# Kernel tuning notes

Hardware: AMD Instinct MI355X
Metric: run time of the kernel (lower is better)

The kernel has to match this reference:

```python
import math
import jax, jax.numpy as jnp
import numpy as np

B = 32        # number of graphs
MAXN = 4096   # nodes per graph (all graphs full)
C = 256       # emb_size_atom
NSEEDS = 409  # int(number_atoms * 0.1)
TOTAL = B * MAXN
INV06 = 1.0 / 0.6
INV_SQRT2 = 1.0 / math.sqrt(2.0)

def scaled_silu(x):
    return jax.nn.silu(x) * INV06

def dense(x, W):
    # Dense(bias=False, activation='silu') == ScaledSiLU(x @ W^T)
    return scaled_silu(x @ W.T)

def res_layer(x, W1, W2):
    return (x + dense(dense(x, W1), W2)) * INV_SQRT2

def layer_norm(x, g, b, eps=1e-5):
    m = jnp.mean(x, -1, keepdims=True)
    v = jnp.var(x, -1, keepdims=True)
    return (x - m) * jax.lax.rsqrt(v + eps) * g + b

def split_heads(x, H):
    # torch.cat(x.split(dV//H, 2), dim=0): head-major stacking on batch axis
    b, n, d = x.shape
    return x.reshape(b, n, H, d // H).transpose(2, 0, 1, 3).reshape(H * b, n, d // H)

def merge_heads(x, H, b):
    _, n, dh = x.shape
    return x.reshape(H, b, n, dh).transpose(1, 2, 0, 3).reshape(b, n, H * dh)

def base_mha(Q, K, Wq, bq, Wk, bk, Wv, bv, Wo, bo, g0, b0, g1, b1, H, mask=None):
    dV = Wq.shape[0]
    Q_ = split_heads(Q @ Wq.T + bq, H)
    K_ = split_heads(K @ Wk.T + bk, H)
    V_ = split_heads(K @ Wv.T + bv, H)
    score = jnp.einsum('bqd,bkd->bqk', Q_, K_) * (1.0 / math.sqrt(dV))
    if mask is not None:
        score = score + jnp.tile(mask, (H, 1, 1))
    A = jax.nn.softmax(score, axis=1)  # FAITHFUL: softmax over the QUERY axis (dim=1 in source)
    out = merge_heads(Q_ + jnp.einsum('bqk,bkd->bqd', A, V_), H, Q.shape[0])
    out = layer_norm(out, g0, b0)
    out = out + jax.nn.relu(out @ Wo.T + bo)
    out = layer_norm(out, g1, b1)
    return out, A

def to_dense_batch(x, batch):
    total = x.shape[0]
    counts = jax.ops.segment_sum(jnp.ones((total,), jnp.int32), batch, num_segments=B)
    offsets = jnp.concatenate([jnp.zeros((1,), jnp.int32), jnp.cumsum(counts)[:-1]])
    pos = jnp.arange(total) - offsets[batch]  # position of each node within its graph
    dense_x = jnp.zeros((B, MAXN, x.shape[-1]), x.dtype).at[batch, pos].set(x)
    omask = jnp.zeros((B, MAXN), bool).at[batch, pos].set(True)
    return dense_x, omask, pos

def _forward(h, batch_seg, W_pre1, W_pre2, S, pWq, pbq, pWk, pbk, pWv, pbv, pWo, pbo, pg0, pb0, pg1, pb1, iWq, ibq, iWk, ibk, iWv, ibv, iWo, ibo, ig0, ib0, ig1, ib1, W_head, W_r1a, W_r1b, W_r2a, W_r2b):
    hres = res_layer(h, W_pre1, W_pre2)
    dx, omask, pos = to_dense_batch(hres, batch_seg)
    mask = jnp.where(omask, 0.0, -1e9).astype(hres.dtype)[:, None, :]  # [B,1,MAXN]
    Q = jnp.tile(S, (B, 1, 1))  # learned seeds [B,NSEEDS,C]
    NAs, A1 = base_mha(Q, dx, pWq, pbq, pWk, pbk, pWv, pbv, pWo, pbo, pg0, pb0, pg1, pb1, 1, mask)
    NAs, _ = base_mha(NAs, NAs, iWq, ibq, iWk, ibk, iWv, ibv, iWo, ibo, ig0, ib0, ig1, ib1, 2, None)
    h_back = jnp.einsum('bsn,bsc->bnc', A1, NAs)  # project back: A1^T @ NAs
    h_up = h_back[batch_seg, pos]                 # flatten back to [TOTAL, C]
    h_up = dense(h_up, W_head)
    h_up = res_layer(h_up, W_r1a, W_r1b)
    h_up = res_layer(h_up, W_r2a, W_r2b)
    return h_up

def setup_inputs() -> dict:
    key = jax.random.key(0)
    ks = jax.random.split(key, 20)
    sc = 1.0 / math.sqrt(C)
    w = lambda k: jax.random.normal(k, (C, C), jnp.float32) * sc
    zb = jnp.zeros((C,), jnp.float32)
    og = jnp.ones((C,), jnp.float32)
    return {
        'h': jax.random.normal(ks[0], (TOTAL, C), jnp.float32),
        'batch_seg': jnp.arange(TOTAL, dtype=jnp.int32) // MAXN,
        'W_pre1': w(ks[1]), 'W_pre2': w(ks[2]),
        'S': jax.random.normal(ks[3], (1, NSEEDS, C), jnp.float32) * math.sqrt(2.0 / (NSEEDS + C)),
        'pWq': w(ks[4]), 'pbq': zb, 'pWk': w(ks[5]), 'pbk': zb,
        'pWv': w(ks[6]), 'pbv': zb, 'pWo': w(ks[7]), 'pbo': zb,
        'pg0': og, 'pb0': zb, 'pg1': og, 'pb1': zb,
        'iWq': w(ks[8]), 'ibq': zb, 'iWk': w(ks[9]), 'ibk': zb,
        'iWv': w(ks[10]), 'ibv': zb, 'iWo': w(ks[11]), 'ibo': zb,
        'ig0': og, 'ib0': zb, 'ig1': og, 'ib1': zb,
        'W_head': w(ks[12]),
        'W_r1a': w(ks[13]), 'W_r1b': w(ks[14]),
        'W_r2a': w(ks[15]), 'W_r2b': w(ks[16]),
    }

def reference(h, batch_seg, W_pre1, W_pre2, S, pWq, pbq, pWk, pbk, pWv, pbv, pWo, pbo, pg0, pb0, pg1, pb1, iWq, ibq, iWk, ibk, iWv, ibv, iWo, ibo, ig0, ib0, ig1, ib1, W_head, W_r1a, W_r1b, W_r2a, W_r2b):
    return _forward(h, batch_seg, W_pre1, W_pre2, S, pWq, pbq, pWk, pbk, pWv, pbv, pWo, pbo, pg0, pb0, pg1, pb1, iWq, ibq, iWk, ibk, iWv, ibv, iWo, ibo, ig0, ib0, ig1, ib1, W_head, W_r1a, W_r1b, W_r2a, W_r2b)
```

## Files before the change

kernel.cpp:

```cpp
#include <hip/hip_runtime.h>


#define BM 128
#define BN 128
#define BKT 32
#define PKM 132
#define XS  264
#define NJOBS 33

typedef __attribute__((ext_vector_type(8))) __bf16 bf16x8;
typedef __attribute__((ext_vector_type(4))) __bf16 bf16x4;
typedef __attribute__((ext_vector_type(4))) float  f32x4;

struct CastJobs {
    const float* src[NJOBS];
    __bf16*      dst[NJOBS];
    long         n[NJOBS];
    int          startBlk[NJOBS];
};

__global__ void cast_many_k(CastJobs J)
{
    int b = blockIdx.x;
    int j = 0;
#pragma unroll
    for (int t = 0; t < NJOBS; t++) { if (J.startBlk[t] <= b) j = t; }
    long idx = ((long)(b - J.startBlk[j]) * 256 + threadIdx.x) * 4;
    if (idx < J.n[j]) {
        f32x4 v = *(const f32x4*)(J.src[j] + idx);
        bf16x4 o;
        o[0] = (__bf16)v[0]; o[1] = (__bf16)v[1];
        o[2] = (__bf16)v[2]; o[3] = (__bf16)v[3];
        *(bf16x4*)(J.dst[j] + idx) = o;
    }
}

__device__ __forceinline__ void gload_lds16(const __bf16* g, __bf16* l)
{
    __builtin_amdgcn_global_load_lds(
        (const __attribute__((address_space(1))) void*)g,
        (__attribute__((address_space(3))) void*)l, 16, 0, 0);
}

__device__ __forceinline__ float ssilu(float v)
{
    float e = __expf(-fabsf(v));
    float sig = (v >= 0.0f) ? 1.0f / (1.0f + e) : e / (1.0f + e);
    return v * sig * 1.6666666666666667f;
}

__device__ __forceinline__ void chain_gemm(const __bf16* __restrict__ Xl,
                                           const __bf16* __restrict__ W,
                                           f32x4 (&acc)[4][4],
                                           int wn, int l15, int lq)
{
#pragma unroll
    for (int i = 0; i < 4; i++)
#pragma unroll
        for (int j = 0; j < 4; j++)
#pragma unroll
            for (int r = 0; r < 4; r++) acc[i][j][r] = 0.0f;
#pragma unroll
    for (int k0 = 0; k0 < 8; k0++) {
        bf16x8 af[4], bfr[4];
#pragma unroll
        for (int i = 0; i < 4; i++)
            af[i] = *(const bf16x8*)(Xl + (i * 16 + l15) * XS + k0 * 32 + lq * 8);
#pragma unroll
        for (int j = 0; j < 4; j++)
            bfr[j] = *(const bf16x8*)(W + (long)(wn + j * 16 + l15) * 256 + k0 * 32 + lq * 8);
#pragma unroll
        for (int i = 0; i < 4; i++)
#pragma unroll
            for (int j = 0; j < 4; j++)
                acc[i][j] = __builtin_amdgcn_mfma_f32_16x16x32_bf16(af[i], bfr[j], acc[i][j], 0, 0, 0);
    }
}

__device__ __forceinline__ void epi_to_lds(const f32x4 (&acc)[4][4],
                                           __bf16* __restrict__ dst,
                                           const __bf16* __restrict__ resL,
                                           int wn, int l15, int lq)
{
#pragma unroll
    for (int i = 0; i < 4; i++)
#pragma unroll
        for (int j = 0; j < 4; j++) {
            int col = wn + j * 16 + l15;
#pragma unroll
            for (int r = 0; r < 4; r++) {
                int row = i * 16 + lq * 4 + r;
                float v = ssilu(acc[i][j][r]);
                if (resL) v = ((float)resL[row * XS + col] + v) * 0.70710678118654752f;
                dst[row * XS + col] = (__bf16)v;
            }
        }
}

__launch_bounds__(256, 2)
__global__ void fuse_front_k(const __bf16* __restrict__ h,
                             const __bf16* __restrict__ Wp1,
                             const __bf16* __restrict__ Wp2,
                             const __bf16* __restrict__ pWk, const __bf16* __restrict__ pbk,
                             const __bf16* __restrict__ pWv, const __bf16* __restrict__ pbv,
                             __bf16* __restrict__ Kb, __bf16* __restrict__ Vt)
{
    __shared__ __align__(16) __bf16 B0[64 * XS];
    __shared__ __align__(16) __bf16 B1[64 * XS];
    const int tid = threadIdx.x, lane = tid & 63, wv = tid >> 6;
    const int wn = wv * 64, l15 = lane & 15, lq = lane >> 4;
    const long row0 = (long)blockIdx.x * 64;

#pragma unroll
    for (int i = 0; i < 8; i++) {
        int v = tid + i * 256;
        int r = v >> 5, kc = (v & 31) * 8;
        *(bf16x8*)(B0 + r * XS + kc) = *(const bf16x8*)(h + (row0 + r) * 256 + kc);
    }
    __syncthreads();

    f32x4 acc[4][4];
    chain_gemm(B0, Wp1, acc, wn, l15, lq);
    epi_to_lds(acc, B1, nullptr, wn, l15, lq);
    __syncthreads();

    chain_gemm(B1, Wp2, acc, wn, l15, lq);
    __syncthreads();
    epi_to_lds(acc, B1, B0, wn, l15, lq);
    __syncthreads();

    chain_gemm(B1, pWk, acc, wn, l15, lq);
#pragma unroll
    for (int i = 0; i < 4; i++)
#pragma unroll
        for (int j = 0; j < 4; j++) {
            int col = wn + j * 16 + l15;
            float bc = (float)pbk[col];
#pragma unroll
            for (int r = 0; r < 4; r++) {
                int row = i * 16 + lq * 4 + r;
                Kb[(row0 + row) * 256 + col] = (__bf16)(acc[i][j][r] + bc);
            }
        }

    chain_gemm(B1, pWv, acc, wn, l15, lq);
    {
        long g   = row0 >> 12;
        long n0g = row0 & 4095;
#pragma unroll
        for (int i = 0; i < 4; i++)
#pragma unroll
            for (int j = 0; j < 4; j++) {
                int col = wn + j * 16 + l15;
                float bc = (float)pbv[col];
                long nb = n0g + i * 16 + lq * 4;
                bf16x4 ov;
#pragma unroll
                for (int r = 0; r < 4; r++) ov[r] = (__bf16)(acc[i][j][r] + bc);
                *(bf16x4*)(Vt + ((g * 256 + col) << 12) + nb) = ov;
            }
    }
}

__launch_bounds__(256, 2)
__global__ void fuse_tail_k(const __bf16* __restrict__ HB,
                            const __bf16* __restrict__ Wh,
                            const __bf16* __restrict__ W1a, const __bf16* __restrict__ W1b,
                            const __bf16* __restrict__ W2a, const __bf16* __restrict__ W2b,
                            float* __restrict__ OUT)
{
    __shared__ __align__(16) __bf16 B0[64 * XS];
    __shared__ __align__(16) __bf16 B1[64 * XS];
    const int tid = threadIdx.x, lane = tid & 63, wv = tid >> 6;
    const int wn = wv * 64, l15 = lane & 15, lq = lane >> 4;
    const long row0 = (long)blockIdx.x * 64;

#pragma unroll
    for (int i = 0; i < 8; i++) {
        int v = tid + i * 256;
        int r = v >> 5, kc = (v & 31) * 8;
        *(bf16x8*)(B0 + r * XS + kc) = *(const bf16x8*)(HB + (row0 + r) * 256 + kc);
    }
    __syncthreads();

    f32x4 acc[4][4];
    chain_gemm(B0, Wh, acc, wn, l15, lq);
    epi_to_lds(acc, B1, nullptr, wn, l15, lq);
    __syncthreads();

    chain_gemm(B1, W1a, acc, wn, l15, lq);
    epi_to_lds(acc, B0, nullptr, wn, l15, lq);
    __syncthreads();

    chain_gemm(B0, W1b, acc, wn, l15, lq);
    __syncthreads();
    epi_to_lds(acc, B0, B1, wn, l15, lq);
    __syncthreads();

    chain_gemm(B0, W2a, acc, wn, l15, lq);
    epi_to_lds(acc, B1, nullptr, wn, l15, lq);
    __syncthreads();

    chain_gemm(B1, W2b, acc, wn, l15, lq);
#pragma unroll
    for (int i = 0; i < 4; i++)
#pragma unroll
        for (int j = 0; j < 4; j++) {
            int col = wn + j * 16 + l15;
#pragma unroll
            for (int r = 0; r < 4; r++) {
                int row = i * 16 + lq * 4 + r;
                float v = ssilu(acc[i][j][r]);
                v = ((float)B0[row * XS + col] + v) * 0.70710678118654752f;
                OUT[(row0 + row) * 256 + col] = v;
            }
        }
}

template<int TRANS>
__device__ __forceinline__ bool stage_load(bf16x8 (&rv)[2], __bf16* __restrict__ lds,
                                           const __bf16* __restrict__ G,
                                           int ld, int r0, int Rg,
                                           int k0, int K, int tid)
{
    if (TRANS == 0) {
        const bool fast = ((ld & 7) == 0) && (r0 + BM <= Rg) && (k0 + BKT <= K);
        if (fast) {
#pragma unroll
            for (int i = 0; i < 2; i++) {
                int v = tid + i * 256;
                int r = v >> 2, kc = (v & 3) * 8;
                gload_lds16(G + (long)(r0 + r) * ld + (k0 + kc), lds + v * 8);
            }
            return true;
        }
#pragma unroll
        for (int i = 0; i < 2; i++) {
            int v = tid + i * 256;
            int r = v >> 2, kc = (v & 3) * 8;
            int gm = r0 + r, gk = k0 + kc;
            bf16x8 val;
#pragma unroll
            for (int j = 0; j < 8; j++) val[j] = (__bf16)0.0f;
            if (gm < Rg) {
                if (((ld & 7) == 0) && (gk + 8 <= K)) {
                    val = *(const bf16x8*)(G + (long)gm * ld + gk);
                } else {
#pragma unroll
                    for (int j = 0; j < 8; j++)
                        if (gk + j < K) val[j] = G[(long)gm * ld + gk + j];
                }
            }
            rv[i] = val;
        }
        return false;
    } else {
#pragma unroll
        for (int i = 0; i < 2; i++) {
            int v = tid + i * 256;
            int kk = v >> 4;
            int mc = (v & 15) * 8;
            int gk = k0 + kk, gm = r0 + mc;
            bf16x8 val;
#pragma unroll
            for (int j = 0; j < 8; j++) val[j] = (__bf16)0.0f;
            if (gk < K) {
                if (((ld & 7) == 0) && (gm + 8 <= Rg)) {
                    val = *(const bf16x8*)(G + (long)gk * ld + gm);
                } else {
#pragma unroll
                    for (int j = 0; j < 8; j++)
                        if (gm + j < Rg) val[j] = G[(long)gk * ld + gm + j];
                }
            }
            rv[i] = val;
        }
        return false;
    }
}

template<int TRANS>
__device__ __forceinline__ void stage_write(const bf16x8 (&rv)[2], __bf16* __restrict__ lds,
                                            int tid, bool fast)
{
    if (TRANS == 0) {
        if (fast) return;
#pragma unroll
        for (int i = 0; i < 2; i++)
            *(bf16x8*)(lds + (tid + i * 256) * 8) = rv[i];
    } else {
#pragma unroll
        for (int i = 0; i < 2; i++) {
            int v = tid + i * 256;
            int kk = v >> 4, mc = (v & 15) * 8;
            bf16x4 lo, hi;
            lo[0] = rv[i][0]; lo[1] = rv[i][1]; lo[2] = rv[i][2]; lo[3] = rv[i][3];
            hi[0] = rv[i][4]; hi[1] = rv[i][5]; hi[2] = rv[i][6]; hi[3] = rv[i][7];
            *(bf16x4*)(lds + kk * PKM + mc)     = lo;
            *(bf16x4*)(lds + kk * PKM + mc + 4) = hi;
        }
    }
}

template<int AT, int BT>
__device__ __forceinline__ void frag_mfma(const __bf16* __restrict__ Ac,
                                          const __bf16* __restrict__ Bc,
                                          f32x4 (&acc)[4][4],
                                          int wm, int wn, int l15, int lq)
{
    bf16x8 af[4], bfr[4];
    if (AT == 0) {
#pragma unroll
        for (int i = 0; i < 4; i++)
            af[i] = *(const bf16x8*)(Ac + (wm + i * 16 + l15) * BKT + lq * 8);
    } else {
#pragma unroll
        for (int i = 0; i < 4; i++) {
            int m = wm + i * 16 + l15;
#pragma unroll
            for (int j = 0; j < 8; j++) af[i][j] = Ac[(lq * 8 + j) * PKM + m];
        }
    }
    if (BT == 1) {
#pragma unroll
        for (int j = 0; j < 4; j++)
            bfr[j] = *(const bf16x8*)(Bc + (wn + j * 16 + l15) * BKT + lq * 8);
    } else {
#pragma unroll
        for (int j = 0; j < 4; j++) {
            int n = wn + j * 16 + l15;
#pragma unroll
            for (int jj = 0; jj < 8; jj++) bfr[j][jj] = Bc[(lq * 8 + jj) * PKM + n];
        }
    }
#pragma unroll
    for (int i = 0; i < 4; i++)
#pragma unroll
        for (int j = 0; j < 4; j++)
            acc[i][j] = __builtin_amdgcn_mfma_f32_16x16x32_bf16(af[i], bfr[j], acc[i][j], 0, 0, 0);
}

template<int AT, int BT, int PIPE>
__launch_bounds__(256, 2)
__global__ void gemm_k(const __bf16* __restrict__ A, long aLo, long aHi, int lda, int Ms,
                       const __bf16* __restrict__ Bm, long bLo, long bHi, int ldb, int Ns,
                       const __bf16* __restrict__ bias,
                       const __bf16* __restrict__ res, long rLo, long rHi, int ldr, int resMode,
                       float* __restrict__ outF, __bf16* __restrict__ outB,
                       long oLo, long oHi, int ldo, int storeT,
                       int M, int N, int K, float oscale, int act)
{
    constexpr int BTT = (BT == 1) ? 0 : 1;
    constexpr int NBUF = PIPE ? 2 : 1;
    __shared__ __align__(16) __bf16 As[NBUF * BKT * PKM];
    __shared__ __align__(16) __bf16 Bs[NBUF * BKT * PKM];

    const int tid = threadIdx.x;
    const int z = blockIdx.z;
    const long zl = (long)(z & 31), zh = (long)(z >> 5);
    const __bf16* Ab = A + zl * aLo + zh * aHi;
    const __bf16* Bb = Bm + zl * bLo + zh * bHi;
    const int m0 = blockIdx.x * BM;
    const int n0 = blockIdx.y * BN;

    f32x4 acc[4][4];
#pragma unroll
    for (int i = 0; i < 4; i++)
#pragma unroll
        for (int j = 0; j < 4; j++)
#pragma unroll
            for (int r = 0; r < 4; r++) acc[i][j][r] = 0.0f;

    const int wv = tid >> 6;
    const int lane = tid & 63;
    const int wm = (wv >> 1) * 64;
    const int wn = (wv & 1) * 64;
    const int l15 = lane & 15;
    const int lq  = lane >> 4;

    if (PIPE == 0) {
        for (int k0 = 0; k0 < K; k0 += BKT) {
            bf16x8 ra[2], rb[2];
            bool fa = stage_load<AT>(ra, As, Ab, lda, m0, Ms, k0, K, tid);
            bool fb = stage_load<BTT>(rb, Bs, Bb, ldb, n0, Ns, k0, K, tid);
            stage_write<AT>(ra, As, tid, fa);
            stage_write<BTT>(rb, Bs, tid, fb);
            __syncthreads();
            frag_mfma<AT, BT>(As, Bs, acc, wm, wn, l15, lq);
            __syncthreads();
        }
    } else {
        constexpr int TSZ = BKT * PKM;
        const int nt = (K + BKT - 1) / BKT;
        bf16x8 ra[2], rb[2];
        bool fa = stage_load<AT>(ra, As, Ab, lda, m0, Ms, 0, K, tid);
        bool fb = stage_load<BTT>(rb, Bs, Bb, ldb, n0, Ns, 0, K, tid);
        stage_write<AT>(ra, As, tid, fa);
        stage_write<BTT>(rb, Bs, tid, fb);
        __syncthreads();
        int cur = 0;
        for (int t = 0; t < nt; t++) {
            const bool nxt = (t + 1 < nt);
            if (nxt) {
                fa = stage_load<AT>(ra, As + (cur ^ 1) * TSZ, Ab, lda, m0, Ms, (t + 1) * BKT, K, tid);
                fb = stage_load<BTT>(rb, Bs + (cur ^ 1) * TSZ, Bb, ldb, n0, Ns, (t + 1) * BKT, K, tid);
            }
            frag_mfma<AT, BT>(As + cur * TSZ, Bs + cur * TSZ, acc, wm, wn, l15, lq);
            if (nxt) {
                stage_write<AT>(ra, As + (cur ^ 1) * TSZ, tid, fa);
                stage_write<BTT>(rb, Bs + (cur ^ 1) * TSZ, tid, fb);
                __syncthreads();
                cur ^= 1;
            }
        }
    }

    const __bf16* Rb = res ? (res + zl * rLo + zh * rHi) : (const __bf16*)nullptr;
    const long ob = zl * oLo + zh * oHi;
#pragma unroll
    for (int i = 0; i < 4; i++) {
#pragma unroll
        for (int j = 0; j < 4; j++) {
            int col = n0 + wn + j * 16 + l15;
            if (col >= N) continue;
            float bcol = bias ? (float)bias[col] : 0.0f;
            int row0 = m0 + wm + i * 16 + lq * 4;
            if (!storeT) {
#pragma unroll
                for (int r = 0; r < 4; r++) {
                    int row = row0 + r;
                    if (row >= M) continue;
                    float v = acc[i][j][r] * oscale + bcol;
                    if (act == 1) v = ssilu(v);
                    else if (act == 2) v = fmaxf(v, 0.0f);
                    if (resMode) {
                        float rv = (float)Rb[(long)row * ldr + col];
                        v = (resMode == 1) ? (rv + v) * 0.70710678118654752f : (rv + v);
                    }
                    long oi = ob + (long)row * ldo + col;
                    if (outF) outF[oi] = v;
                    else      outB[oi] = (__bf16)v;
                }
            } else {
                if (row0 + 3 < M) {
                    bf16x4 rv4;
                    if (resMode) rv4 = *(const bf16x4*)(Rb + (long)col * ldr + row0);
                    float vs[4];
#pragma unroll
                    for (int r = 0; r < 4; r++) {
                        float v = acc[i][j][r] * oscale + bcol;
                        if (act == 1) v = ssilu(v);
                        else if (act == 2) v = fmaxf(v, 0.0f);
                        if (resMode) {
                            float rv = (float)rv4[r];
                            v = (resMode == 1) ? (rv + v) * 0.70710678118654752f : (rv + v);
                        }
                        vs[r] = v;
                    }
                    if (outF) {
                        f32x4 o4; o4[0] = vs[0]; o4[1] = vs[1]; o4[2] = vs[2]; o4[3] = vs[3];
                        *(f32x4*)(outF + ob + (long)col * ldo + row0) = o4;
                    } else {
                        bf16x4 ov;
                        ov[0] = (__bf16)vs[0]; ov[1] = (__bf16)vs[1];
                        ov[2] = (__bf16)vs[2]; ov[3] = (__bf16)vs[3];
                        *(bf16x4*)(outB + ob + (long)col * ldo + row0) = ov;
                    }
                } else {
#pragma unroll
                    for (int r = 0; r < 4; r++) {
                        int row = row0 + r;
                        if (row >= M) continue;
                        float v = acc[i][j][r] * oscale + bcol;
                        if (act == 1) v = ssilu(v);
                        else if (act == 2) v = fmaxf(v, 0.0f);
                        if (resMode) {
                            float rv = (float)Rb[(long)col * ldr + row];
                            v = (resMode == 1) ? (rv + v) * 0.70710678118654752f : (rv + v);
                        }
                        if (outF) outF[ob + (long)col * ldo + row] = v;
                        else      outB[ob + (long)col * ldo + row] = (__bf16)v;
                    }
                }
            }
        }
    }
}

__global__ void reduce4_k(const float* __restrict__ P, const __bf16* __restrict__ Qp,
                          __bf16* __restrict__ out)
{
    long idx = (long)blockIdx.x * 256 + threadIdx.x;
    long g = idx / (409 * 64);
    long r = idx - g * (409 * 64);
    long s = r >> 6;
    int  c4 = (int)(r & 63) * 4;
    long base = (g * 409 + s) * 256 + c4;
    const long SP = 32L * 409 * 256;
    f32x4 a0 = *(const f32x4*)(P + base);
    f32x4 a1 = *(const f32x4*)(P + base + SP);
    f32x4 a2 = *(const f32x4*)(P + base + 2 * SP);
    f32x4 a3 = *(const f32x4*)(P + base + 3 * SP);
    bf16x4 q = *(const bf16x4*)(Qp + s * 256 + c4);
    bf16x4 o;
#pragma unroll
    for (int k = 0; k < 4; k++)
        o[k] = (__bf16)(a0[k] + a1[k] + a2[k] + a3[k] + (float)q[k]);
    *(bf16x4*)(out + base) = o;
}

__global__ void rowsoftmax_k(const float* __restrict__ S, __bf16* __restrict__ A,
                             long rows, int L, int ldS, int ldA, int Lw)
{
    long row = (long)blockIdx.x * 4 + (threadIdx.x >> 6);
    if (row >= rows) return;
    int lane = threadIdx.x & 63;
    const float* Sr = S + row * (long)ldS;
    float v[7];
    int cnt = 0;
    for (int q = lane; q < L; q += 64) v[cnt++] = Sr[q];
    float m = -3.0e38f;
    for (int c = 0; c < cnt; c++) m = fmaxf(m, v[c]);
#pragma unroll
    for (int off = 32; off > 0; off >>= 1) m = fmaxf(m, __shfl_xor(m, off));
    float s = 0.0f;
    for (int c = 0; c < cnt; c++) s += __expf(v[c] - m);
#pragma unroll
    for (int off = 32; off > 0; off >>= 1) s += __shfl_xor(s, off);
    float inv = 1.0f / s;
    cnt = 0;
    for (int q = lane; q < Lw; q += 64) {
        float o = 0.0f;
        if (q < L) { o = __expf(v[cnt] - m) * inv; cnt++; }
        A[row * (long)ldA + q] = (__bf16)o;
    }
}

__global__ void ln_k(const __bf16* __restrict__ X, __bf16* __restrict__ Y,
                     const __bf16* __restrict__ gamma, const __bf16* __restrict__ beta,
                     int rows)
{
    int row = blockIdx.x * 4 + (threadIdx.x >> 6);
    if (row >= rows) return;
    int lane = threadIdx.x & 63;
    bf16x4 xv = *(const bf16x4*)(X + (long)row * 256 + lane * 4);
    float v0 = (float)xv[0], v1 = (float)xv[1], v2 = (float)xv[2], v3 = (float)xv[3];
    float s = v0 + v1 + v2 + v3;
#pragma unroll
    for (int off = 32; off > 0; off >>= 1) s += __shfl_xor(s, off);
    float mean = s * (1.0f / 256.0f);
    float d0 = v0 - mean, d1 = v1 - mean, d2 = v2 - mean, d3 = v3 - mean;
    float q = d0 * d0 + d1 * d1 + d2 * d2 + d3 * d3;
#pragma unroll
    for (int off = 32; off > 0; off >>= 1) q += __shfl_xor(q, off);
    float sc = rsqrtf(q * (1.0f / 256.0f) + 1e-5f);
    bf16x4 gv = *(const bf16x4*)(gamma + lane * 4);
    bf16x4 bv = *(const bf16x4*)(beta + lane * 4);
    bf16x4 ov;
    ov[0] = (__bf16)(d0 * sc * (float)gv[0] + (float)bv[0]);
    ov[1] = (__bf16)(d1 * sc * (float)gv[1] + (float)bv[1]);
    ov[2] = (__bf16)(d2 * sc * (float)gv[2] + (float)bv[2]);
    ov[3] = (__bf16)(d3 * sc * (float)gv[3] + (float)bv[3]);
    *(bf16x4*)(Y + (long)row * 256 + lane * 4) = ov;
}

__global__ void sentinel_k(float* out, long n)
{
    long i = (long)blockIdx.x * blockDim.x + threadIdx.x;
    if (i < n) out[i] = 12345.0f;
}

static void G(hipStream_t st, int AT, int BT,
              const __bf16* A, long aLo, long aHi, int lda, int Ms,
              const __bf16* B, long bLo, long bHi, int ldb, int Ns,
              const __bf16* bias,
              const __bf16* res, long rLo, long rHi, int ldr, int resMode,
              float* outF, __bf16* outB, long oLo, long oHi, int ldo, int storeT,
              int M, int N, int K, int Z, float oscale, int act)
{
    dim3 grid((M + BM - 1) / BM, (N + BN - 1) / BN, Z), blk(256, 1, 1);
#define GARGS A, aLo, aHi, lda, Ms, B, bLo, bHi, ldb, Ns, bias, res, rLo, rHi, ldr, resMode, \
              outF, outB, oLo, oHi, ldo, storeT, M, N, K, oscale, act
    if (AT == 0 && BT == 1) {
        gemm_k<0, 1, 0><<<grid, blk, 0, st>>>(GARGS);
    } else if (AT == 0 && BT == 0) {
        if (K >= 512) gemm_k<0, 0, 1><<<grid, blk, 0, st>>>(GARGS);
        else          gemm_k<0, 0, 0><<<grid, blk, 0, st>>>(GARGS);
    } else {
        gemm_k<1, 0, 0><<<grid, blk, 0, st>>>(GARGS);
    }
#undef GARGS
}

extern "C" void kernel_launch(void* const* d_in, const int* in_sizes, int n_in,
                              void* d_out, int out_size, void* d_ws, size_t ws_size,
                              hipStream_t stream)
{
    (void)in_sizes; (void)n_in;
    float* OUT = (float*)d_out;

    const int TOT = 131072, NC = 256, NS = 409, MX = 4096;
    const int NSP = 416;
    const int NSB = 32 * NS;
    const long NTC = (long)TOT * NC;
    const int GCH = 4;

    static const int  pidx[NJOBS] = {0,2,3,4,5,6,7,8,9,10,11,12,13,14,15,16,
                                     17,18,19,20,21,22,23,24,25,26,27,28,29,30,31,32,33};
    static const long pn[NJOBS]   = {33554432,65536,65536,104704,
                                     65536,256,65536,256,65536,256,65536,256,
                                     256,256,256,256,
                                     65536,256,65536,256,65536,256,65536,256,
                                     256,256,256,256,
                                     65536,65536,65536,65536,65536};
    long ptot = 0;
    for (int j = 0; j < NJOBS; j++) ptot += pn[j];

    char* w = (char*)d_ws;
    size_t off = 0;
    auto take = [&](size_t bytes) -> char* {
        char* p = w + off;
        off += (bytes + 255) & ~(size_t)255;
        return p;
    };
    char* pblk = take((size_t)ptot * 2);
    char* reg0 = take((size_t)64 * NS * NSP * 4);
    char* reg1 = take((size_t)32 * MX * NSP * 2);
    char* reg2 = take((size_t)NTC * 2);
    char* reg3 = take((size_t)NTC * 2);
    __bf16* QP  = (__bf16*)take((size_t)NS * NC * 2);
    __bf16* sb0 = (__bf16*)take((size_t)NSB * NC * 2);
    __bf16* sb1 = (__bf16*)take((size_t)NSB * NC * 2);
    __bf16* sb2 = (__bf16*)take((size_t)NSB * NC * 2);
    __bf16* sb3 = (__bf16*)take((size_t)NSB * NC * 2);
    __bf16* sb4 = (__bf16*)take((size_t)NSB * NC * 2);
    __bf16* sb5 = (__bf16*)take((size_t)NSB * NC * 2);

    if (off > ws_size) {
        long n = out_size;
        sentinel_k<<<(int)((n + 255) / 256), 256, 0, stream>>>(OUT, n);
        return;
    }

    CastJobs J;
    __bf16* P[NJOBS];
    {
        long cum = 0;
        int blk = 0;
        for (int j = 0; j < NJOBS; j++) {
            J.src[j] = (const float*)d_in[pidx[j]];
            P[j] = (__bf16*)pblk + cum;
            J.dst[j] = P[j];
            J.n[j] = pn[j];
            J.startBlk[j] = blk;
            blk += (int)((pn[j] + 1023) / 1024);
            cum += pn[j];
        }
        cast_many_k<<<blk, 256, 0, stream>>>(J);
    }
    const __bf16 *hB = P[0], *Wpre1 = P[1], *Wpre2 = P[2], *Sseed = P[3];
    const __bf16 *pWq = P[4], *pbq = P[5], *pWk = P[6], *pbk = P[7];
    const __bf16 *pWv = P[8], *pbv = P[9], *pWo = P[10], *pbo = P[11];
    const __bf16 *pg0 = P[12], *pb0 = P[13], *pg1 = P[14], *pb1 = P[15];
    const __bf16 *iWq = P[16], *ibq = P[17], *iWk = P[18], *ibk = P[19];
    const __bf16 *iWv = P[20], *ibv = P[21], *iWo = P[22], *ibo = P[23];
    const __bf16 *ig0 = P[24], *ib0 = P[25], *ig1 = P[26], *ib1 = P[27];
    const __bf16 *Whead = P[28], *Wr1a = P[29], *Wr1b = P[30];
    const __bf16 *Wr2a = P[31], *Wr2b = P[32];

    float*  STs = (float*)reg0;
    float*  S2T = (float*)reg0;
    __bf16* A1T = (__bf16*)reg1;
    __bf16* Kb  = (__bf16*)reg2;
    float*  PP  = (float*)reg2;
    __bf16* HB  = (__bf16*)reg2;
    __bf16* Vt  = (__bf16*)reg3;
    __bf16* A2T = (__bf16*)reg3;

    fuse_front_k<<<dim3(TOT / 64), 256, 0, stream>>>(hB, Wpre1, Wpre2,
                                                     pWk, pbk, pWv, pbv, Kb, Vt);
    G(stream, 0, 1, Sseed, 0, 0, 256, NS, pWq, 0, 0, 256, 256, pbq,
      nullptr, 0, 0, 0, 0, nullptr, QP, 0, 0, 256, 0, NS, 256, 256, 1, 1.0f, 0);
    for (int c = 0; c < 32 / GCH; c++) {
        const __bf16* Kc = Kb + (size_t)c * GCH * MX * NC;
        G(stream, 0, 1, Kc, (long)MX * NC, 0, 256, MX, QP, 0, 0, 256, NS, nullptr,
          nullptr, 0, 0, 0, 0, STs, nullptr, (long)MX * NSP, 0, NSP, 0,
          MX, NS, 256, GCH, 0.0625f, 0);
        rowsoftmax_k<<<dim3(GCH * MX / 4), 256, 0, stream>>>(
            STs, A1T + (size_t)c * GCH * MX * NSP, (long)GCH * MX, NS, NSP, NSP, NSP);
    }
    G(stream, 0, 0, Vt, (long)NC * MX, 1024, MX, NC,
      A1T, (long)MX * NSP, 1024L * NSP, NSP, NSP, nullptr,
      nullptr, 0, 0, 0, 0, PP, nullptr, (long)NS * NC, 32L * NS * NC, NC, 1,
      NC, NS, 1024, 128, 1.0f, 0);
    reduce4_k<<<dim3((unsigned)((32L * NS * 64) / 256)), 256, 0, stream>>>(PP, QP, sb0);
    ln_k<<<dim3(NSB / 4), 256, 0, stream>>>(sb0, sb1, pg0, pb0, NSB);
    G(stream, 0, 1, sb1, 0, 0, 256, NSB, pWo, 0, 0, 256, 256, pbo,
      sb1, 0, 0, 256, 2, nullptr, sb2, 0, 0, 256, 0, NSB, 256, 256, 1, 1.0f, 2);
    ln_k<<<dim3(NSB / 4), 256, 0, stream>>>(sb2, sb0, pg1, pb1, NSB);
    G(stream, 0, 1, sb0, 0, 0, 256, NSB, iWq, 0, 0, 256, 256, ibq,
      nullptr, 0, 0, 0, 0, nullptr, sb1, 0, 0, 256, 0, NSB, 256, 256, 1, 1.0f, 0);
    G(stream, 0, 1, sb0, 0, 0, 256, NSB, iWk, 0, 0, 256, 256, ibk,
      nullptr, 0, 0, 0, 0, nullptr, sb2, 0, 0, 256, 0, NSB, 256, 256, 1, 1.0f, 0);
    G(stream, 0, 1, sb0, 0, 0, 256, NSB, iWv, 0, 0, 256, 256, ibv,
      nullptr, 0, 0, 0, 0, nullptr, sb3, 0, 0, 256, 0, NSB, 256, 256, 1, 1.0f, 0);
    G(stream, 0, 1, sb2, (long)NS * NC, 128, 256, NS, sb1, (long)NS * NC, 128, 256, NS, nullptr,
      nullptr, 0, 0, 0, 0, S2T, nullptr, (long)NS * NSP, 32L * NS * NSP, NSP, 0,
      NS, NS, 128, 64, 0.0625f, 0);
    rowsoftmax_k<<<dim3(64 * NS / 4), 256, 0, stream>>>(S2T, A2T, 64L * NS, NS, NSP, NSP, NSP);
    G(stream, 1, 0, A2T, (long)NS * NSP, 32L * NS * NSP, NSP, NSP,
      sb3, (long)NS * NC, 128, 256, 128, nullptr,
      sb1, (long)NS * NC, 128, 256, 2, nullptr, sb4, (long)NS * NC, 128, 256, 0,
      NS, 128, NS, 64, 1.0f, 0);
    ln_k<<<dim3(NSB / 4), 256, 0, stream>>>(sb4, sb5, ig0, ib0, NSB);
    G(stream, 0, 1, sb5, 0, 0, 256, NSB, iWo, 0, 0, 256, 256, ibo,
      sb5, 0, 0, 256, 2, nullptr, sb4, 0, 0, 256, 0, NSB, 256, 256, 1, 1.0f, 2);
    ln_k<<<dim3(NSB / 4), 256, 0, stream>>>(sb4, sb1, ig1, ib1, NSB);
    G(stream, 0, 0, A1T, (long)MX * NSP, 0, NSP, MX, sb1, (long)NS * NC, 0, 256, 256, nullptr,
      nullptr, 0, 0, 0, 0, nullptr, HB, (long)MX * NC, 0, 256, 0, MX, 256, 416, 32, 1.0f, 0);
    fuse_tail_k<<<dim3(TOT / 64), 256, 0, stream>>>(HB, Whead, Wr1a, Wr1b,
                                                    Wr2a, Wr2b, OUT);
}
```

Baseline: 1.483 ms.

## Transpose chain GEMM operands for vectorized epilogues and register-held residuals

Adds a transposed chain GEMM variant where weights are the A operand, so each lane's accumulator holds four consecutive output columns. Epilogues can then use packed bf16x4 LDS and global stores and f32x4 output writes instead of scalar stores. Residuals in the head kernel are kept in registers rather than reread from LDS, which removes one barrier and an in-place residual pass. ScaledSiLU is simplified to a single exp plus a hardware reciprocal, which can lose accuracy or overflow for large negative inputs. The extra register arrays could raise register pressure under the launch bounds of two blocks per SIMD.

```diff
diff --git a/kernel.cpp b/kernel.cpp
--- a/kernel.cpp
+++ b/kernel.cpp
@@ -44,9 +44,36 @@
 
 __device__ __forceinline__ float ssilu(float v)
 {
-    float e = __expf(-fabsf(v));
-    float sig = (v >= 0.0f) ? 1.0f / (1.0f + e) : e / (1.0f + e);
-    return v * sig * 1.6666666666666667f;
+    float ex = __expf(-v);
+    return v * __builtin_amdgcn_rcpf(1.0f + ex) * 1.6666666666666667f;
+}
+
+__device__ __forceinline__ void chain_gemmT(const __bf16* __restrict__ Xl,
+                                            const __bf16* __restrict__ W,
+                                            f32x4 (&acc)[4][4],
+                                            int wn, int l15, int lq)
+{
+#pragma unroll
+    for (int i = 0; i < 4; i++)
+#pragma unroll
+        for (int j = 0; j < 4; j++)
+#pragma unroll
+            for (int r = 0; r < 4; r++) acc[i][j][r] = 0.0f;
+#pragma unroll
+    for (int k0 = 0; k0 < 8; k0++) {
+        bf16x8 wf[4], xf[4];
+#pragma unroll
+        for (int i = 0; i < 4; i++)
+            wf[i] = *(const bf16x8*)(W + (long)(wn + i * 16 + l15) * 256 + k0 * 32 + lq * 8);
+#pragma unroll
+        for (int j = 0; j < 4; j++)
+            xf[j] = *(const bf16x8*)(Xl + (j * 16 + l15) * XS + k0 * 32 + lq * 8);
+#pragma unroll
+        for (int i = 0; i < 4; i++)
+#pragma unroll
+            for (int j = 0; j < 4; j++)
+                acc[i][j] = __builtin_amdgcn_mfma_f32_16x16x32_bf16(wf[i], xf[j], acc[i][j], 0, 0, 0);
+    }
 }
 
 __device__ __forceinline__ void chain_gemm(const __bf16* __restrict__ Xl,
@@ -75,26 +102,6 @@
             for (int j = 0; j < 4; j++)
                 acc[i][j] = __builtin_amdgcn_mfma_f32_16x16x32_bf16(af[i], bfr[j], acc[i][j], 0, 0, 0);
     }
-}
-
-__device__ __forceinline__ void epi_to_lds(const f32x4 (&acc)[4][4],
-                                           __bf16* __restrict__ dst,
-                                           const __bf16* __restrict__ resL,
-                                           int wn, int l15, int lq)
-{
-#pragma unroll
-    for (int i = 0; i < 4; i++)
-#pragma unroll
-        for (int j = 0; j < 4; j++) {
-            int col = wn + j * 16 + l15;
-#pragma unroll
-            for (int r = 0; r < 4; r++) {
-                int row = i * 16 + lq * 4 + r;
-                float v = ssilu(acc[i][j][r]);
-                if (resL) v = ((float)resL[row * XS + col] + v) * 0.70710678118654752f;
-                dst[row * XS + col] = (__bf16)v;
-            }
-        }
 }
 
 __launch_bounds__(256, 2)
@@ -120,30 +127,54 @@
     __syncthreads();
 
     f32x4 acc[4][4];
-    chain_gemm(B0, Wp1, acc, wn, l15, lq);
-    epi_to_lds(acc, B1, nullptr, wn, l15, lq);
+    chain_gemmT(B0, Wp1, acc, wn, l15, lq);
+#pragma unroll
+    for (int j = 0; j < 4; j++) {
+        int r = j * 16 + l15;
+#pragma unroll
+        for (int i = 0; i < 4; i++) {
+            int c0 = wn + i * 16 + lq * 4;
+            bf16x4 o;
+#pragma unroll
+            for (int t = 0; t < 4; t++) o[t] = (__bf16)ssilu(acc[i][j][t]);
+            *(bf16x4*)(B1 + r * XS + c0) = o;
+        }
+    }
     __syncthreads();
 
-    chain_gemm(B1, Wp2, acc, wn, l15, lq);
+    chain_gemmT(B1, Wp2, acc, wn, l15, lq);
+#pragma unroll
+    for (int j = 0; j < 4; j++) {
+        int r = j * 16 + l15;
+#pragma unroll
+        for (int i = 0; i < 4; i++) {
+            int c0 = wn + i * 16 + lq * 4;
+            bf16x4 hv = *(const bf16x4*)(B0 + r * XS + c0);
+            bf16x4 o;
+#pragma unroll
+            for (int t = 0; t < 4; t++)
+                o[t] = (__bf16)(((float)hv[t] + ssilu(acc[i][j][t])) * 0.70710678118654752f);
+            *(bf16x4*)(B0 + r * XS + c0) = o;
+        }
+    }
     __syncthreads();
-    epi_to_lds(acc, B1, B0, wn, l15, lq);
-    __syncthreads();
-
-    chain_gemm(B1, pWk, acc, wn, l15, lq);
-#pragma unroll
-    for (int i = 0; i < 4; i++)
-#pragma unroll
-        for (int j = 0; j < 4; j++) {
-            int col = wn + j * 16 + l15;
-            float bc = (float)pbk[col];
-#pragma unroll
-            for (int r = 0; r < 4; r++) {
-                int row = i * 16 + lq * 4 + r;
-                Kb[(row0 + row) * 256 + col] = (__bf16)(acc[i][j][r] + bc);
-            }
-        }
-
-    chain_gemm(B1, pWv, acc, wn, l15, lq);
+
+    chain_gemmT(B0, pWk, acc, wn, l15, lq);
+#pragma unroll
+    for (int j = 0; j < 4; j++) {
+        int r = j * 16 + l15;
+#pragma unroll
+        for (int i = 0; i < 4; i++) {
+            int c0 = wn + i * 16 + lq * 4;
+            bf16x4 bb = *(const bf16x4*)(pbk + c0);
+            bf16x4 o;
+#pragma unroll
+            for (int t = 0; t < 4; t++) o[t] = (__bf16)(acc[i][j][t] + (float)bb[t]);
+            *(bf16x4*)(Kb + (row0 + r) * 256 + c0) = o;
+        }
+    }
+
+    chain_gemm(B0, pWv, acc, wn, l15, lq);
     {
         long g   = row0 >> 12;
         long n0g = row0 & 4095;
@@ -184,37 +215,85 @@
     __syncthreads();
 
     f32x4 acc[4][4];
-    chain_gemm(B0, Wh, acc, wn, l15, lq);
-    epi_to_lds(acc, B1, nullptr, wn, l15, lq);
+    bf16x4 tres[4][4], ures[4][4];
+
+    chain_gemmT(B0, Wh, acc, wn, l15, lq);
+#pragma unroll
+    for (int j = 0; j < 4; j++) {
+        int r = j * 16 + l15;
+#pragma unroll
+        for (int i = 0; i < 4; i++) {
+            int c0 = wn + i * 16 + lq * 4;
+            bf16x4 o;
+#pragma unroll
+            for (int t = 0; t < 4; t++) o[t] = (__bf16)ssilu(acc[i][j][t]);
+            tres[i][j] = o;
+            *(bf16x4*)(B1 + r * XS + c0) = o;
+        }
+    }
     __syncthreads();
 
-    chain_gemm(B1, W1a, acc, wn, l15, lq);
-    epi_to_lds(acc, B0, nullptr, wn, l15, lq);
+    chain_gemmT(B1, W1a, acc, wn, l15, lq);
+#pragma unroll
+    for (int j = 0; j < 4; j++) {
+        int r = j * 16 + l15;
+#pragma unroll
+        for (int i = 0; i < 4; i++) {
+            int c0 = wn + i * 16 + lq * 4;
+            bf16x4 o;
+#pragma unroll
+            for (int t = 0; t < 4; t++) o[t] = (__bf16)ssilu(acc[i][j][t]);
+            *(bf16x4*)(B0 + r * XS + c0) = o;
+        }
+    }
     __syncthreads();
 
-    chain_gemm(B0, W1b, acc, wn, l15, lq);
+    chain_gemmT(B0, W1b, acc, wn, l15, lq);
+#pragma unroll
+    for (int j = 0; j < 4; j++) {
+        int r = j * 16 + l15;
+#pragma unroll
+        for (int i = 0; i < 4; i++) {
+            int c0 = wn + i * 16 + lq * 4;
+            bf16x4 o;
+#pragma unroll
+            for (int t = 0; t < 4; t++)
+                o[t] = (__bf16)(((float)tres[i][j][t] + ssilu(acc[i][j][t])) * 0.70710678118654752f);
+            ures[i][j] = o;
+            *(bf16x4*)(B1 + r * XS + c0) = o;
+        }
+    }
     __syncthreads();
-    epi_to_lds(acc, B0, B1, wn, l15, lq);
+
+    chain_gemmT(B1, W2a, acc, wn, l15, lq);
+#pragma unroll
+    for (int j = 0; j < 4; j++) {
+        int r = j * 16 + l15;
+#pragma unroll
+        for (int i = 0; i < 4; i++) {
+            int c0 = wn + i * 16 + lq * 4;
+            bf16x4 o;
+#pragma unroll
+            for (int t = 0; t < 4; t++) o[t] = (__bf16)ssilu(acc[i][j][t]);
+            *(bf16x4*)(B0 + r * XS + c0) = o;
+        }
+    }
     __syncthreads();
 
-    chain_gemm(B0, W2a, acc, wn, l15, lq);
-    epi_to_lds(acc, B1, nullptr, wn, l15, lq);
-    __syncthreads();
-
-    chain_gemm(B1, W2b, acc, wn, l15, lq);
-#pragma unroll
-    for (int i = 0; i < 4; i++)
-#pragma unroll
-        for (int j = 0; j < 4; j++) {
-            int col = wn + j * 16 + l15;
-#pragma unroll
-            for (int r = 0; r < 4; r++) {
-                int row = i * 16 + lq * 4 + r;
-                float v = ssilu(acc[i][j][r]);
-                v = ((float)B0[row * XS + col] + v) * 0.70710678118654752f;
-                OUT[(row0 + row) * 256 + col] = v;
-            }
-        }
+    chain_gemmT(B0, W2b, acc, wn, l15, lq);
+#pragma unroll
+    for (int j = 0; j < 4; j++) {
+        int r = j * 16 + l15;
+#pragma unroll
+        for (int i = 0; i < 4; i++) {
+            int c0 = wn + i * 16 + lq * 4;
+            f32x4 ov;
+#pragma unroll
+            for (int t = 0; t < 4; t++)
+                ov[t] = ((float)ures[i][j][t] + ssilu(acc[i][j][t])) * 0.70710678118654752f;
+            *(f32x4*)(OUT + (row0 + r) * 256 + c0) = ov;
+        }
+    }
 }
 
 template<int TRANS>
```

Measured after the change: 1.442 ms. 1.03x faster.
